# Performance work log

Measured on AMD Instinct MI355X. Metric: run time of the kernel, lower is better.

Reference implementation:

```python
import jax, jax.numpy as jnp
import numpy as np
import math

D_MODEL = 96
D_STATE = 16
D_CONV = 3
EXPAND = 2
D_INNER = EXPAND * D_MODEL          # 192
DT_RANK = math.ceil(D_MODEL / 16)   # 6
B_SZ, H_SZ, W_SZ = 2, 56, 56


def setup_inputs() -> dict:
    key = jax.random.key(0)
    ks = jax.random.split(key, 10)
    x = jax.random.normal(ks[0], (B_SZ, H_SZ, W_SZ, D_MODEL), jnp.float32)
    W_in = jax.random.normal(ks[1], (D_MODEL, 2 * D_INNER), jnp.float32) * 0.02
    conv_w = jax.random.normal(ks[2], (D_CONV, D_CONV, 1, D_INNER), jnp.float32) * 0.1
    conv_b = jax.random.normal(ks[3], (D_INNER,), jnp.float32) * 0.02
    W_xproj = jax.random.normal(ks[4], (D_INNER, DT_RANK + 2 * D_STATE), jnp.float32) * 0.02
    dt_std = DT_RANK ** -0.5
    W_dt = jax.random.uniform(ks[5], (DT_RANK, D_INNER), jnp.float32, -dt_std, dt_std)
    # dt_proj bias init: inverse-softplus of dt ~ LogUniform(dt_min, dt_max)
    dt_min, dt_max = 1e-3, 1e-1
    dt = jnp.exp(jax.random.uniform(ks[6], (D_INNER,), jnp.float32)
                 * (math.log(dt_max) - math.log(dt_min)) + math.log(dt_min))
    dt = jnp.clip(dt, 1e-4, None)
    b_dt = dt + jnp.log(-jnp.expm1(-dt))
    # A_log initialized to broadcast arange(1..d_state) (as in the source, no log taken)
    A_log = jnp.tile(jnp.arange(1, D_STATE + 1, dtype=jnp.float32)[None, :], (D_INNER, 1))
    D_skip = jnp.ones((D_INNER,), jnp.float32)
    W_out = jax.random.normal(ks[7], (D_INNER, D_MODEL), jnp.float32) * 0.02
    return {"x": x, "W_in": W_in, "conv_w": conv_w, "conv_b": conv_b,
            "W_xproj": W_xproj, "W_dt": W_dt, "b_dt": b_dt,
            "A_log": A_log, "D_skip": D_skip, "W_out": W_out}


def _selective_scan(xs, dt, A, Bm, Cm, D_skip):
    """Canonical Mamba selective scan.
    xs, dt: (G, L, C); Bm, Cm: (G, L, N); A: (C, N); D_skip: (C,).
    h_l = exp(dt_l * A) * h_{l-1} + dt_l * B_l * x_l ;  y_l = <h_l, C_l> + D * x_l
    """
    dA = jnp.exp(dt[..., None] * A)                              # (G,L,C,N)
    dBx = dt[..., None] * Bm[:, :, None, :] * xs[..., None]      # (G,L,C,N)

    def step(h, inp):
        dA_l, dBx_l, C_l = inp                                   # (G,C,N),(G,C,N),(G,N)
        h = dA_l * h + dBx_l
        y = jnp.einsum('gcn,gn->gc', h, C_l)
        return h, y

    G, L, C = xs.shape
    h0 = jnp.zeros((G, C, D_STATE), xs.dtype)
    _, ys = jax.lax.scan(step, h0, (jnp.moveaxis(dA, 1, 0),
                                    jnp.moveaxis(dBx, 1, 0),
                                    jnp.moveaxis(Cm, 1, 0)))
    ys = jnp.moveaxis(ys, 0, 1)                                  # (G,L,C)
    return ys + D_skip * xs


def reference(x, W_in, conv_w, conv_b, W_xproj, W_dt, b_dt, A_log, D_skip, W_out):
    B, H, W, _ = x.shape  # H == W required (source sums transposed scans directly)
    xz = x @ W_in                                                # (B,H,W,2*d_inner)
    xm, z = jnp.split(xz, 2, axis=-1)
    pad = (D_CONV - 1) // 2
    xm = jax.lax.conv_general_dilated(
        xm, conv_w, (1, 1), [(pad, pad), (pad, pad)],
        dimension_numbers=('NHWC', 'HWIO', 'NHWC'),
        feature_group_count=D_INNER) + conv_b                    # depthwise conv
    # 4 scan directions
    xt = jnp.swapaxes(xm, 1, 2)
    xs4 = jnp.stack([xm, jnp.flip(xm, 2), xt, jnp.flip(xt, 1)], 0)  # (4,B,H,W,C)
    G, L = 4 * B, H * W
    xs = xs4.reshape(G, L, D_INNER)
    x_dbl = xs @ W_xproj                                          # (G,L,dt_rank+2N)
    dtr, Bm, Cm = jnp.split(x_dbl, [DT_RANK, DT_RANK + D_STATE], axis=-1)
    dt = jax.nn.softplus(dtr @ W_dt + b_dt)                       # (G,L,d_inner)
    A = -jnp.exp(A_log)                                           # (d_inner, N)
    ys = _selective_scan(xs, dt, A, Bm, Cm, D_skip)               # (G,L,d_inner)
    y = ys.reshape(4, B, H, W, D_INNER).sum(0)                    # sum 4 directions
    y = jax.nn.silu(z) * y
    return y @ W_out                                              # (B,H,W,d_model)
```

## Files before the change

kernel.cpp:

```cpp
#include <hip/hip_runtime.h>
#include <math.h>

#define NPIX 6272
#define LVAL 3136
#define CIN 192
#define NST 16
#define HW 56

__device__ __forceinline__ float softplusf(float v) {
    return (v > 20.0f) ? v : log1pf(expf(v));
}

__device__ __forceinline__ void dir_geom(int d, int b, int& si, int& sj, int& off) {
    if (d == 0)      { si = HW;  sj = 1;   off = b * LVAL; }
    else if (d == 1) { si = HW;  sj = -1;  off = b * LVAL + (HW - 1); }
    else if (d == 2) { si = 1;   sj = HW;  off = b * LVAL; }
    else             { si = -1;  sj = HW;  off = b * LVAL + (HW - 1); }
}

__global__ __launch_bounds__(384) void k_inproj(
    const float* __restrict__ x, const float* __restrict__ W_in,
    float* __restrict__ xm, float* __restrict__ z)
{
    __shared__ __align__(16) float xs[96][20];
    const int p0 = blockIdx.x * 16;
    const int t = threadIdx.x;
    for (int e = t; e < 16 * 96; e += 384) {
        int p = e / 96, kk = e % 96;
        xs[kk][p] = x[p0 * 96 + e];
    }
    __syncthreads();
    float acc[16];
#pragma unroll
    for (int p = 0; p < 16; ++p) acc[p] = 0.f;
    for (int k = 0; k < 96; ++k) {
        float w = W_in[k * 384 + t];
        float4 x0 = *(const float4*)&xs[k][0];
        float4 x1 = *(const float4*)&xs[k][4];
        float4 x2 = *(const float4*)&xs[k][8];
        float4 x3 = *(const float4*)&xs[k][12];
        acc[0]  = fmaf(x0.x, w, acc[0]);  acc[1]  = fmaf(x0.y, w, acc[1]);
        acc[2]  = fmaf(x0.z, w, acc[2]);  acc[3]  = fmaf(x0.w, w, acc[3]);
        acc[4]  = fmaf(x1.x, w, acc[4]);  acc[5]  = fmaf(x1.y, w, acc[5]);
        acc[6]  = fmaf(x1.z, w, acc[6]);  acc[7]  = fmaf(x1.w, w, acc[7]);
        acc[8]  = fmaf(x2.x, w, acc[8]);  acc[9]  = fmaf(x2.y, w, acc[9]);
        acc[10] = fmaf(x2.z, w, acc[10]); acc[11] = fmaf(x2.w, w, acc[11]);
        acc[12] = fmaf(x3.x, w, acc[12]); acc[13] = fmaf(x3.y, w, acc[13]);
        acc[14] = fmaf(x3.z, w, acc[14]); acc[15] = fmaf(x3.w, w, acc[15]);
    }
#pragma unroll
    for (int p = 0; p < 16; ++p) {
        int pix = p0 + p;
        if (t < 192) xm[pix * CIN + t] = acc[p];
        else         z[pix * CIN + (t - 192)] = acc[p];
    }
}

__global__ __launch_bounds__(256) void k_conv(
    const float* __restrict__ xm, const float* __restrict__ cw,
    const float* __restrict__ cb, float* __restrict__ xcv)
{
    int e = blockIdx.x * 256 + threadIdx.x;
    if (e >= NPIX * CIN) return;
    int c = e % CIN;
    int pix = e / CIN;
    int w = pix % HW;
    int rest = pix / HW;
    int h = rest % HW;
    int b = rest / HW;
    float acc = cb[c];
#pragma unroll
    for (int ky = 0; ky < 3; ++ky) {
        int hh = h + ky - 1;
        if (hh < 0 || hh >= HW) continue;
#pragma unroll
        for (int kx = 0; kx < 3; ++kx) {
            int ww = w + kx - 1;
            if (ww < 0 || ww >= HW) continue;
            acc = fmaf(xm[((b * HW + hh) * HW + ww) * CIN + c],
                       cw[(ky * 3 + kx) * CIN + c], acc);
        }
    }
    xcv[e] = acc;
}

__global__ __launch_bounds__(256) void k_xproj_dt(
    const float* __restrict__ xcv, const float* __restrict__ W_xproj,
    const float* __restrict__ W_dt, const float* __restrict__ b_dt,
    float* __restrict__ Bp, float* __restrict__ Cp, float* __restrict__ dtp)
{
    __shared__ __align__(16) float xs[192][28];
    __shared__ float dtr_lds[24][8];
    const int p0 = blockIdx.x * 24;
    const int t = threadIdx.x;
    for (int e = t; e < 24 * 192; e += 256) {
        int p = e / 192, kk = e % 192;
        int pix = p0 + p;
        xs[kk][p] = (pix < NPIX) ? xcv[pix * CIN + kk] : 0.f;
    }
    __syncthreads();
    const int j  = t % 40;
    const int pq = t / 40;
    if (pq < 6) {
        const int jc = (j < 38) ? j : 37;
        float a0 = 0.f, a1 = 0.f, a2 = 0.f, a3 = 0.f;
        for (int k = 0; k < 192; ++k) {
            float w = W_xproj[k * 38 + jc];
            float4 xv = *(const float4*)&xs[k][pq * 4];
            a0 = fmaf(xv.x, w, a0); a1 = fmaf(xv.y, w, a1);
            a2 = fmaf(xv.z, w, a2); a3 = fmaf(xv.w, w, a3);
        }
        if (j < 38) {
            float r[4] = {a0, a1, a2, a3};
#pragma unroll
            for (int q = 0; q < 4; ++q) {
                int p = pq * 4 + q;
                int pix = p0 + p;
                if (j < 6) dtr_lds[p][j] = r[q];
                if (pix < NPIX) {
                    if (j < 6)       ;
                    else if (j < 22) Bp[pix * NST + (j - 6)] = r[q];
                    else             Cp[pix * NST + (j - 22)] = r[q];
                }
            }
        }
    }
    __syncthreads();
    for (int e = t; e < 24 * 192; e += 256) {
        int p = e / 192, c = e % 192;
        int pix = p0 + p;
        if (pix >= NPIX) continue;
        float v = b_dt[c];
#pragma unroll
        for (int r = 0; r < 6; ++r)
            v = fmaf(dtr_lds[p][r], W_dt[r * CIN + c], v);
        dtp[pix * CIN + c] = softplusf(v);
    }
}

template<int CHUNK>
__global__ __launch_bounds__(384) void k_scan_p1(
    const float* __restrict__ xcv, const float* __restrict__ dtp,
    const float* __restrict__ Bp, const float* __restrict__ A_log,
    float* __restrict__ Pbuf, float* __restrict__ qbuf)
{
    constexpr int CPR = HW / CHUNK;
    __shared__ __align__(16) float Bs[CHUNK * NST];
    const int g = blockIdx.y;
    const int k = blockIdx.x;
    const int t = threadIdx.x;
    const int wv = t >> 6;
    const int lane = t & 63;
    const int cl = lane & 31, nh = lane >> 5;
    const int c = wv * 32 + cl;
    const int n0 = nh * 8;
    const int d = g >> 1, b = g & 1;
    int si, sj, off;
    dir_geom(d, b, si, sj, off);
    const int base = off + (k / CPR) * si + ((k % CPR) * CHUNK) * sj;

    for (int e = t; e < CHUNK * NST; e += 384) {
        int jj = e >> 4, n = e & 15;
        Bs[e] = Bp[(base + jj * sj) * NST + n];
    }

    const float LOG2E = 1.4426950408889634f;
    float a2[8];
    {
        const float4* Ar = (const float4*)(A_log + c * NST + n0);
#pragma unroll
        for (int q = 0; q < 2; ++q) {
            float4 v = Ar[q];
            a2[q*4+0] = -expf(v.x) * LOG2E;
            a2[q*4+1] = -expf(v.y) * LOG2E;
            a2[q*4+2] = -expf(v.z) * LOG2E;
            a2[q*4+3] = -expf(v.w) * LOG2E;
        }
    }
    __syncthreads();

    float h[8];
#pragma unroll
    for (int i = 0; i < 8; ++i) h[i] = 0.f;
    float Sdt = 0.f;

    float dt_v = dtp[base * CIN + c];
    float x_v  = xcv[base * CIN + c];
    for (int jj = 0; jj < CHUNK; ++jj) {
        float dt_c = dt_v, x_c = x_v;
        int jn = (jj + 1 < CHUNK) ? jj + 1 : jj;
        int pixn = base + jn * sj;
        dt_v = dtp[pixn * CIN + c];
        x_v  = xcv[pixn * CIN + c];
        float dtx = dt_c * x_c;
        Sdt += dt_c;
        float Bv[8];
        {
            const float4* Brow = (const float4*)(Bs + jj * NST + n0);
            float4 t0 = Brow[0], t1 = Brow[1];
            Bv[0]=t0.x; Bv[1]=t0.y; Bv[2]=t0.z; Bv[3]=t0.w;
            Bv[4]=t1.x; Bv[5]=t1.y; Bv[6]=t1.z; Bv[7]=t1.w;
        }
#pragma unroll
        for (int i = 0; i < 8; ++i) {
            float dA = exp2f(dt_c * a2[i]);
            h[i] = fmaf(dA, h[i], dtx * Bv[i]);
        }
    }
    float P[8];
#pragma unroll
    for (int i = 0; i < 8; ++i) P[i] = exp2f(a2[i] * Sdt);

    float4* Pd = (float4*)(Pbuf + ((size_t)(k * 8 + g) * CIN + c) * NST + n0);
    float4* qd = (float4*)(qbuf + ((size_t)(k * 8 + g) * CIN + c) * NST + n0);
    Pd[0] = make_float4(P[0], P[1], P[2], P[3]);
    Pd[1] = make_float4(P[4], P[5], P[6], P[7]);
    qd[0] = make_float4(h[0], h[1], h[2], h[3]);
    qd[1] = make_float4(h[4], h[5], h[6], h[7]);
}

__global__ __launch_bounds__(256) void k_scan_fix(
    const float* __restrict__ Pbuf, float* __restrict__ qbuf, int nch)
{
    const int g = blockIdx.y;
    const int lo = blockIdx.x * 256 + threadIdx.x;
    const size_t stride = (size_t)8 * CIN * NST;
    size_t idx  = (size_t)g * CIN * NST + lo;
    size_t pidx = idx;
    float Pr[8], qr[8];
#pragma unroll
    for (int i = 0; i < 8; ++i) { Pr[i] = Pbuf[pidx]; qr[i] = qbuf[pidx]; pidx += stride; }
    float h = 0.f;
    for (int k = 0; k < nch; k += 8) {
        float Pn[8], qn[8];
        if (k + 8 < nch) {
#pragma unroll
            for (int i = 0; i < 8; ++i) {
                Pn[i] = Pbuf[pidx + (size_t)i * stride];
                qn[i] = qbuf[pidx + (size_t)i * stride];
            }
        } else {
#pragma unroll
            for (int i = 0; i < 8; ++i) { Pn[i] = 0.f; qn[i] = 0.f; }
        }
#pragma unroll
        for (int i = 0; i < 8; ++i) {
            qbuf[idx] = h;
            h = fmaf(Pr[i], h, qr[i]);
            idx += stride;
        }
#pragma unroll
        for (int i = 0; i < 8; ++i) { Pr[i] = Pn[i]; qr[i] = qn[i]; }
        pidx += (size_t)8 * stride;
    }
}

template<int CHUNK>
__global__ __launch_bounds__(384) void k_scan_p2(
    const float* __restrict__ xcv, const float* __restrict__ dtp,
    const float* __restrict__ Bp, const float* __restrict__ Cp,
    const float* __restrict__ A_log, const float* __restrict__ D_skip,
    const float* __restrict__ qbuf, float* __restrict__ Y4)
{
    constexpr int CPR = HW / CHUNK;
    __shared__ __align__(16) float Bs[CHUNK * NST];
    __shared__ __align__(16) float Cs[CHUNK * NST];
    const int g = blockIdx.y;
    const int k = blockIdx.x;
    const int t = threadIdx.x;
    const int wv = t >> 6;
    const int lane = t & 63;
    const int cl = lane & 31, nh = lane >> 5;
    const int c = wv * 32 + cl;
    const int n0 = nh * 8;
    const int d = g >> 1, b = g & 1;
    int si, sj, off;
    dir_geom(d, b, si, sj, off);
    const int base = off + (k / CPR) * si + ((k % CPR) * CHUNK) * sj;

    for (int e = t; e < CHUNK * NST; e += 384) {
        int jj = e >> 4, n = e & 15;
        int pa = (base + jj * sj) * NST + n;
        Bs[e] = Bp[pa];
        Cs[e] = Cp[pa];
    }

    const float LOG2E = 1.4426950408889634f;
    float a2[8];
    {
        const float4* Ar = (const float4*)(A_log + c * NST + n0);
#pragma unroll
        for (int q = 0; q < 2; ++q) {
            float4 v = Ar[q];
            a2[q*4+0] = -expf(v.x) * LOG2E;
            a2[q*4+1] = -expf(v.y) * LOG2E;
            a2[q*4+2] = -expf(v.z) * LOG2E;
            a2[q*4+3] = -expf(v.w) * LOG2E;
        }
    }
    const float Dc = D_skip[c];

    float h[8];
    {
        const float4* qd = (const float4*)(qbuf + ((size_t)(k * 8 + g) * CIN + c) * NST + n0);
        float4 v0 = qd[0], v1 = qd[1];
        h[0]=v0.x; h[1]=v0.y; h[2]=v0.z; h[3]=v0.w;
        h[4]=v1.x; h[5]=v1.y; h[6]=v1.z; h[7]=v1.w;
    }
    __syncthreads();

    float* yo = Y4 + ((size_t)d * NPIX + (size_t)b * LVAL + (size_t)k * CHUNK) * CIN;

    float dt_v = dtp[base * CIN + c];
    float x_v  = xcv[base * CIN + c];
    for (int jj = 0; jj < CHUNK; ++jj) {
        float dt_c = dt_v, x_c = x_v;
        int jn = (jj + 1 < CHUNK) ? jj + 1 : jj;
        int pixn = base + jn * sj;
        dt_v = dtp[pixn * CIN + c];
        x_v  = xcv[pixn * CIN + c];
        float dtx = dt_c * x_c;
        float Bv[8], Cv[8];
        {
            const float4* Brow = (const float4*)(Bs + jj * NST + n0);
            const float4* Crow = (const float4*)(Cs + jj * NST + n0);
            float4 t0 = Brow[0], t1 = Brow[1];
            float4 u0 = Crow[0], u1 = Crow[1];
            Bv[0]=t0.x; Bv[1]=t0.y; Bv[2]=t0.z; Bv[3]=t0.w;
            Bv[4]=t1.x; Bv[5]=t1.y; Bv[6]=t1.z; Bv[7]=t1.w;
            Cv[0]=u0.x; Cv[1]=u0.y; Cv[2]=u0.z; Cv[3]=u0.w;
            Cv[4]=u1.x; Cv[5]=u1.y; Cv[6]=u1.z; Cv[7]=u1.w;
        }
        float yc0 = 0.f, yc1 = 0.f;
#pragma unroll
        for (int i = 0; i < 8; i += 2) {
            float dA0 = exp2f(dt_c * a2[i]);
            float dA1 = exp2f(dt_c * a2[i+1]);
            h[i]   = fmaf(dA0, h[i],   dtx * Bv[i]);
            h[i+1] = fmaf(dA1, h[i+1], dtx * Bv[i+1]);
            yc0 = fmaf(h[i],   Cv[i],   yc0);
            yc1 = fmaf(h[i+1], Cv[i+1], yc1);
        }
        float yc = yc0 + yc1;
        yc += __shfl_xor(yc, 32, 64);
        if (nh == 0)
            yo[jj * CIN + c] = fmaf(Dc, x_c, yc);
    }
}

__global__ __launch_bounds__(192) void k_gateout(
    const float* __restrict__ Y4, const float* __restrict__ z,
    const float* __restrict__ W_out, float* __restrict__ out)
{
    __shared__ __align__(16) float xs[192][20];
    const int p0 = blockIdx.x * 16;
    const int t = threadIdx.x;
    const size_t NP = (size_t)NPIX * CIN;
#pragma unroll
    for (int i = 0; i < 16; ++i) {
        size_t idx = (size_t)(p0 + i) * CIN + t;
        float s = Y4[idx] + Y4[idx + NP] + Y4[idx + 2 * NP] + Y4[idx + 3 * NP];
        float zz = z[idx];
        float sig = 1.f / (1.f + expf(-zz));
        xs[t][i] = zz * sig * s;
    }
    __syncthreads();
    const int j  = t % 96;
    const int ph = t / 96;
    float acc[8];
#pragma unroll
    for (int p = 0; p < 8; ++p) acc[p] = 0.f;
    for (int k = 0; k < 192; ++k) {
        float w = W_out[k * 96 + j];
        float4 x0 = *(const float4*)&xs[k][ph * 8];
        float4 x1 = *(const float4*)&xs[k][ph * 8 + 4];
        acc[0] = fmaf(x0.x, w, acc[0]); acc[1] = fmaf(x0.y, w, acc[1]);
        acc[2] = fmaf(x0.z, w, acc[2]); acc[3] = fmaf(x0.w, w, acc[3]);
        acc[4] = fmaf(x1.x, w, acc[4]); acc[5] = fmaf(x1.y, w, acc[5]);
        acc[6] = fmaf(x1.z, w, acc[6]); acc[7] = fmaf(x1.w, w, acc[7]);
    }
#pragma unroll
    for (int p = 0; p < 8; ++p)
        out[(p0 + ph * 8 + p) * 96 + j] = acc[p];
}

template<int CHUNK>
static void launch_scan(const float* xcv, const float* dtp, const float* Bp,
                        const float* Cp, const float* A_log, const float* D_skip,
                        float* Pbuf, float* qbuf, float* Y4, hipStream_t stream)
{
    const int nch = LVAL / CHUNK;
    k_scan_p1<CHUNK><<<dim3(nch, 8), 384, 0, stream>>>(xcv, dtp, Bp, A_log, Pbuf, qbuf);
    k_scan_fix<<<dim3(12, 8), 256, 0, stream>>>(Pbuf, qbuf, nch);
    k_scan_p2<CHUNK><<<dim3(nch, 8), 384, 0, stream>>>(xcv, dtp, Bp, Cp, A_log, D_skip, qbuf, Y4);
}

extern "C" void kernel_launch(void* const* d_in, const int* in_sizes, int n_in,
                              void* d_out, int out_size, void* d_ws, size_t ws_size,
                              hipStream_t stream) {
    const float* x      = (const float*)d_in[0];
    const float* W_in   = (const float*)d_in[1];
    const float* conv_w = (const float*)d_in[2];
    const float* conv_b = (const float*)d_in[3];
    const float* W_xproj= (const float*)d_in[4];
    const float* W_dt   = (const float*)d_in[5];
    const float* b_dt   = (const float*)d_in[6];
    const float* A_log  = (const float*)d_in[7];
    const float* D_skip = (const float*)d_in[8];
    const float* W_out  = (const float*)d_in[9];
    float* out = (float*)d_out;

    float* ws  = (float*)d_ws;
    float* xm  = ws;
    float* z   = xm  + NPIX * CIN;
    float* xcv = z   + NPIX * CIN;
    float* dtp = xcv + NPIX * CIN;
    float* Bp  = dtp + NPIX * CIN;
    float* Cp  = Bp  + NPIX * NST;
    float* Y4  = Cp  + NPIX * NST;
    float* Pbuf= Y4  + (size_t)4 * NPIX * CIN;

    const size_t base_fl = 9834496;
    const size_t ws_fl = ws_size / 4;
    int chunk;
    if (ws_fl >= base_fl + (size_t)2 * 112 * 24576) chunk = 28;
    else                                            chunk = 56;
    float* qbuf = Pbuf + (size_t)(LVAL / chunk) * 8 * CIN * NST;

    k_inproj  <<<NPIX / 16, 384, 0, stream>>>(x, W_in, xm, z);
    k_conv    <<<(NPIX * CIN) / 256, 256, 0, stream>>>(xm, conv_w, conv_b, xcv);
    k_xproj_dt<<<(NPIX + 23) / 24, 256, 0, stream>>>(xcv, W_xproj, W_dt, b_dt, Bp, Cp, dtp);
    if (chunk == 28) launch_scan<28>(xcv, dtp, Bp, Cp, A_log, D_skip, Pbuf, qbuf, Y4, stream);
    else             launch_scan<56>(xcv, dtp, Bp, Cp, A_log, D_skip, Pbuf, qbuf, Y4, stream);
    k_gateout <<<NPIX / 16, 192, 0, stream>>>(Y4, z, W_out, out);
}
```

Measured before the change: 214.0 us.

## Interleave dt and x into float2 buffer, split-K xproj, widen gateout blocks

After: 207.3 us. 3.2% less time.

```diff
diff --git a/kernel.cpp b/kernel.cpp
--- a/kernel.cpp
+++ b/kernel.cpp
@@ -84,49 +84,58 @@
     xcv[e] = acc;
 }
 
-__global__ __launch_bounds__(256) void k_xproj_dt(
+__global__ __launch_bounds__(512) void k_xproj_dt(
     const float* __restrict__ xcv, const float* __restrict__ W_xproj,
     const float* __restrict__ W_dt, const float* __restrict__ b_dt,
-    float* __restrict__ Bp, float* __restrict__ Cp, float* __restrict__ dtp)
+    float* __restrict__ Bp, float* __restrict__ Cp, float2* __restrict__ dtx2)
 {
     __shared__ __align__(16) float xs[192][28];
+    __shared__ float part[2][24][40];
     __shared__ float dtr_lds[24][8];
     const int p0 = blockIdx.x * 24;
     const int t = threadIdx.x;
-    for (int e = t; e < 24 * 192; e += 256) {
+    for (int e = t; e < 24 * 192; e += 512) {
         int p = e / 192, kk = e % 192;
         int pix = p0 + p;
         xs[kk][p] = (pix < NPIX) ? xcv[pix * CIN + kk] : 0.f;
     }
     __syncthreads();
-    const int j  = t % 40;
-    const int pq = t / 40;
+    const int th = t & 255;
+    const int kh = t >> 8;
+    const int j  = th % 40;
+    const int pq = th / 40;
     if (pq < 6) {
         const int jc = (j < 38) ? j : 37;
         float a0 = 0.f, a1 = 0.f, a2 = 0.f, a3 = 0.f;
-        for (int k = 0; k < 192; ++k) {
+        const int k0 = kh * 96;
+        for (int k = k0; k < k0 + 96; ++k) {
             float w = W_xproj[k * 38 + jc];
             float4 xv = *(const float4*)&xs[k][pq * 4];
             a0 = fmaf(xv.x, w, a0); a1 = fmaf(xv.y, w, a1);
             a2 = fmaf(xv.z, w, a2); a3 = fmaf(xv.w, w, a3);
         }
-        if (j < 38) {
-            float r[4] = {a0, a1, a2, a3};
-#pragma unroll
-            for (int q = 0; q < 4; ++q) {
-                int p = pq * 4 + q;
-                int pix = p0 + p;
-                if (j < 6) dtr_lds[p][j] = r[q];
-                if (pix < NPIX) {
-                    if (j < 6)       ;
-                    else if (j < 22) Bp[pix * NST + (j - 6)] = r[q];
-                    else             Cp[pix * NST + (j - 22)] = r[q];
-                }
+        part[kh][pq * 4 + 0][j] = a0;
+        part[kh][pq * 4 + 1][j] = a1;
+        part[kh][pq * 4 + 2][j] = a2;
+        part[kh][pq * 4 + 3][j] = a3;
+    }
+    __syncthreads();
+    if (kh == 0 && pq < 6 && j < 38) {
+#pragma unroll
+        for (int q = 0; q < 4; ++q) {
+            int p = pq * 4 + q;
+            float r = part[0][p][j] + part[1][p][j];
+            int pix = p0 + p;
+            if (j < 6) dtr_lds[p][j] = r;
+            if (pix < NPIX) {
+                if (j < 6)       ;
+                else if (j < 22) Bp[pix * NST + (j - 6)] = r;
+                else             Cp[pix * NST + (j - 22)] = r;
             }
         }
     }
     __syncthreads();
-    for (int e = t; e < 24 * 192; e += 256) {
+    for (int e = t; e < 24 * 192; e += 512) {
         int p = e / 192, c = e % 192;
         int pix = p0 + p;
         if (pix >= NPIX) continue;
@@ -134,14 +143,14 @@
 #pragma unroll
         for (int r = 0; r < 6; ++r)
             v = fmaf(dtr_lds[p][r], W_dt[r * CIN + c], v);
-        dtp[pix * CIN + c] = softplusf(v);
+        dtx2[(size_t)pix * CIN + c] = make_float2(softplusf(v), xs[c][p]);
     }
 }
 
 template<int CHUNK>
 __global__ __launch_bounds__(384) void k_scan_p1(
-    const float* __restrict__ xcv, const float* __restrict__ dtp,
-    const float* __restrict__ Bp, const float* __restrict__ A_log,
+    const float2* __restrict__ dtx2, const float* __restrict__ Bp,
+    const float* __restrict__ A_log,
     float* __restrict__ Pbuf, float* __restrict__ qbuf)
 {
     constexpr int CPR = HW / CHUNK;
@@ -184,14 +193,11 @@
     for (int i = 0; i < 8; ++i) h[i] = 0.f;
     float Sdt = 0.f;
 
-    float dt_v = dtp[base * CIN + c];
-    float x_v  = xcv[base * CIN + c];
+    float2 dv = dtx2[(size_t)base * CIN + c];
     for (int jj = 0; jj < CHUNK; ++jj) {
-        float dt_c = dt_v, x_c = x_v;
+        float dt_c = dv.x, x_c = dv.y;
         int jn = (jj + 1 < CHUNK) ? jj + 1 : jj;
-        int pixn = base + jn * sj;
-        dt_v = dtp[pixn * CIN + c];
-        x_v  = xcv[pixn * CIN + c];
+        dv = dtx2[(size_t)(base + jn * sj) * CIN + c];
         float dtx = dt_c * x_c;
         Sdt += dt_c;
         float Bv[8];
@@ -257,9 +263,9 @@
 
 template<int CHUNK>
 __global__ __launch_bounds__(384) void k_scan_p2(
-    const float* __restrict__ xcv, const float* __restrict__ dtp,
-    const float* __restrict__ Bp, const float* __restrict__ Cp,
-    const float* __restrict__ A_log, const float* __restrict__ D_skip,
+    const float2* __restrict__ dtx2, const float* __restrict__ Bp,
+    const float* __restrict__ Cp, const float* __restrict__ A_log,
+    const float* __restrict__ D_skip,
     const float* __restrict__ qbuf, float* __restrict__ Y4)
 {
     constexpr int CPR = HW / CHUNK;
@@ -311,14 +317,11 @@
 
     float* yo = Y4 + ((size_t)d * NPIX + (size_t)b * LVAL + (size_t)k * CHUNK) * CIN;
 
-    float dt_v = dtp[base * CIN + c];
-    float x_v  = xcv[base * CIN + c];
+    float2 dv = dtx2[(size_t)base * CIN + c];
     for (int jj = 0; jj < CHUNK; ++jj) {
-        float dt_c = dt_v, x_c = x_v;
+        float dt_c = dv.x, x_c = dv.y;
         int jn = (jj + 1 < CHUNK) ? jj + 1 : jj;
-        int pixn = base + jn * sj;
-        dt_v = dtp[pixn * CIN + c];
-        x_v  = xcv[pixn * CIN + c];
+        dv = dtx2[(size_t)(base + jn * sj) * CIN + c];
         float dtx = dt_c * x_c;
         float Bv[8], Cv[8];
         {
@@ -348,7 +351,7 @@
     }
 }
 
-__global__ __launch_bounds__(192) void k_gateout(
+__global__ __launch_bounds__(384) void k_gateout(
     const float* __restrict__ Y4, const float* __restrict__ z,
     const float* __restrict__ W_out, float* __restrict__ out)
 {
@@ -356,43 +359,38 @@
     const int p0 = blockIdx.x * 16;
     const int t = threadIdx.x;
     const size_t NP = (size_t)NPIX * CIN;
-#pragma unroll
-    for (int i = 0; i < 16; ++i) {
-        size_t idx = (size_t)(p0 + i) * CIN + t;
+    for (int e = t; e < 16 * 192; e += 384) {
+        int p = e / 192, c = e % 192;
+        size_t idx = (size_t)(p0 + p) * CIN + c;
         float s = Y4[idx] + Y4[idx + NP] + Y4[idx + 2 * NP] + Y4[idx + 3 * NP];
         float zz = z[idx];
         float sig = 1.f / (1.f + expf(-zz));
-        xs[t][i] = zz * sig * s;
+        xs[c][p] = zz * sig * s;
     }
     __syncthreads();
     const int j  = t % 96;
     const int ph = t / 96;
-    float acc[8];
-#pragma unroll
-    for (int p = 0; p < 8; ++p) acc[p] = 0.f;
+    float acc[4] = {0.f, 0.f, 0.f, 0.f};
     for (int k = 0; k < 192; ++k) {
         float w = W_out[k * 96 + j];
-        float4 x0 = *(const float4*)&xs[k][ph * 8];
-        float4 x1 = *(const float4*)&xs[k][ph * 8 + 4];
-        acc[0] = fmaf(x0.x, w, acc[0]); acc[1] = fmaf(x0.y, w, acc[1]);
-        acc[2] = fmaf(x0.z, w, acc[2]); acc[3] = fmaf(x0.w, w, acc[3]);
-        acc[4] = fmaf(x1.x, w, acc[4]); acc[5] = fmaf(x1.y, w, acc[5]);
-        acc[6] = fmaf(x1.z, w, acc[6]); acc[7] = fmaf(x1.w, w, acc[7]);
-    }
-#pragma unroll
-    for (int p = 0; p < 8; ++p)
-        out[(p0 + ph * 8 + p) * 96 + j] = acc[p];
+        float4 xv = *(const float4*)&xs[k][ph * 4];
+        acc[0] = fmaf(xv.x, w, acc[0]); acc[1] = fmaf(xv.y, w, acc[1]);
+        acc[2] = fmaf(xv.z, w, acc[2]); acc[3] = fmaf(xv.w, w, acc[3]);
+    }
+#pragma unroll
+    for (int p = 0; p < 4; ++p)
+        out[(p0 + ph * 4 + p) * 96 + j] = acc[p];
 }
 
 template<int CHUNK>
-static void launch_scan(const float* xcv, const float* dtp, const float* Bp,
-                        const float* Cp, const float* A_log, const float* D_skip,
+static void launch_scan(const float2* dtx2, const float* Bp, const float* Cp,
+                        const float* A_log, const float* D_skip,
                         float* Pbuf, float* qbuf, float* Y4, hipStream_t stream)
 {
     const int nch = LVAL / CHUNK;
-    k_scan_p1<CHUNK><<<dim3(nch, 8), 384, 0, stream>>>(xcv, dtp, Bp, A_log, Pbuf, qbuf);
+    k_scan_p1<CHUNK><<<dim3(nch, 8), 384, 0, stream>>>(dtx2, Bp, A_log, Pbuf, qbuf);
     k_scan_fix<<<dim3(12, 8), 256, 0, stream>>>(Pbuf, qbuf, nch);
-    k_scan_p2<CHUNK><<<dim3(nch, 8), 384, 0, stream>>>(xcv, dtp, Bp, Cp, A_log, D_skip, qbuf, Y4);
+    k_scan_p2<CHUNK><<<dim3(nch, 8), 384, 0, stream>>>(dtx2, Bp, Cp, A_log, D_skip, qbuf, Y4);
 }
 
 extern "C" void kernel_launch(void* const* d_in, const int* in_sizes, int n_in,
@@ -410,17 +408,17 @@
     const float* W_out  = (const float*)d_in[9];
     float* out = (float*)d_out;
 
-    float* ws  = (float*)d_ws;
-    float* xm  = ws;
-    float* z   = xm  + NPIX * CIN;
-    float* xcv = z   + NPIX * CIN;
-    float* dtp = xcv + NPIX * CIN;
-    float* Bp  = dtp + NPIX * CIN;
-    float* Cp  = Bp  + NPIX * NST;
-    float* Y4  = Cp  + NPIX * NST;
-    float* Pbuf= Y4  + (size_t)4 * NPIX * CIN;
-
-    const size_t base_fl = 9834496;
+    float* ws   = (float*)d_ws;
+    float* xm   = ws;
+    float* z    = xm  + NPIX * CIN;
+    float* xcv  = z   + NPIX * CIN;
+    float2* dtx2= (float2*)(xcv + NPIX * CIN);
+    float* Bp   = (float*)(dtx2 + (size_t)NPIX * CIN);
+    float* Cp   = Bp  + NPIX * NST;
+    float* Y4   = Cp  + NPIX * NST;
+    float* Pbuf = Y4  + (size_t)4 * NPIX * CIN;
+
+    const size_t base_fl = 11038720;
     const size_t ws_fl = ws_size / 4;
     int chunk;
     if (ws_fl >= base_fl + (size_t)2 * 112 * 24576) chunk = 28;
@@ -429,8 +427,8 @@
 
     k_inproj  <<<NPIX / 16, 384, 0, stream>>>(x, W_in, xm, z);
     k_conv    <<<(NPIX * CIN) / 256, 256, 0, stream>>>(xm, conv_w, conv_b, xcv);
-    k_xproj_dt<<<(NPIX + 23) / 24, 256, 0, stream>>>(xcv, W_xproj, W_dt, b_dt, Bp, Cp, dtp);
-    if (chunk == 28) launch_scan<28>(xcv, dtp, Bp, Cp, A_log, D_skip, Pbuf, qbuf, Y4, stream);
-    else             launch_scan<56>(xcv, dtp, Bp, Cp, A_log, D_skip, Pbuf, qbuf, Y4, stream);
-    k_gateout <<<NPIX / 16, 192, 0, stream>>>(Y4, z, W_out, out);
-}
+    k_xproj_dt<<<(NPIX + 23) / 24, 512, 0, stream>>>(xcv, W_xproj, W_dt, b_dt, Bp, Cp, dtx2);
+    if (chunk == 28) launch_scan<28>(dtx2, Bp, Cp, A_log, D_skip, Pbuf, qbuf, Y4, stream);
+    else             launch_scan<56>(dtx2, Bp, Cp, A_log, D_skip, Pbuf, qbuf, Y4, stream);
+    k_gateout <<<NPIX / 16, 384, 0, stream>>>(Y4, z, W_out, out);
+}
```
